# Kernel tuning notes

Hardware: AMD Instinct MI355X
Metric: run time of the kernel (lower is better)

The kernel has to match this reference:

```python
import jax, jax.numpy as jnp
import numpy as np

N, E, D, L, G = 100000, 300000, 256, 5, 4096


def _bn(x, p):
    # p: [4, dim] = (gamma, beta, running_mean, running_var); eval-mode BatchNorm1d
    g, b, m, v = p
    return (x - m) * jax.lax.rsqrt(v + 1e-5) * g + b


def setup_inputs() -> dict:
    key = jax.random.key(0)
    ks = iter(jax.random.split(key, 48))

    def nrm(shape, scale=0.02):
        return jax.random.normal(next(ks), shape, dtype=jnp.float32) * scale

    def bn_params(n, dim):
        g = 1.0 + nrm((n, dim), 0.1)
        b = nrm((n, dim), 0.1)
        m = nrm((n, dim), 0.1)
        v = 1.0 + jax.random.uniform(next(ks), (n, dim), dtype=jnp.float32)
        return jnp.stack([g, b, m, v], axis=1)  # [n,4,dim]

    return {
        "x": jax.random.randint(next(ks), (N, 9), 0, 2, dtype=jnp.int32),
        "edge_index": jax.random.randint(next(ks), (2, E), 0, N, dtype=jnp.int32),
        "edge_attr": jax.random.randint(next(ks), (E, 3), 0, 2, dtype=jnp.int32),
        "batch": jnp.sort(jax.random.randint(next(ks), (N,), 0, G, dtype=jnp.int32)),
        "atom_emb": nrm((9, 120, D)),            # AtomEncoder: 9 feature tables
        "bond_emb": nrm((L, 3, 6, D)),           # per-layer BondEncoder: 3 feature tables
        "vn0": jnp.zeros((D,), jnp.float32),     # virtualnode embedding (init 0)
        "eps": jnp.zeros((L,), jnp.float32),     # GIN eps per layer
        "conv_W1": nrm((L, D, 2 * D), 1.0 / np.sqrt(D)),     # GIN MLP (sampled BayesLinear)
        "conv_b1": nrm((L, 2 * D)),
        "conv_bn1": bn_params(L, 2 * D),
        "conv_W2": nrm((L, 2 * D, D), 1.0 / np.sqrt(2 * D)),
        "conv_b2": nrm((L, D)),
        "node_bn": bn_params(L, D),              # per-layer outer BatchNorm
        "vn_W1": nrm((L - 1, D, D), 1.0 / np.sqrt(D)),       # virtual-node MLP
        "vn_b1": nrm((L - 1, D)),
        "vn_bn1": bn_params(L - 1, D),
        "vn_W2": nrm((L - 1, D, D), 1.0 / np.sqrt(D)),
        "vn_b2": nrm((L - 1, D)),
        "vn_bn2": bn_params(L - 1, D),
    }


def reference(x, edge_index, edge_attr, batch, atom_emb, bond_emb, vn0, eps,
              conv_W1, conv_b1, conv_bn1, conv_W2, conv_b2, node_bn,
              vn_W1, vn_b1, vn_bn1, vn_W2, vn_b2, vn_bn2):
    src, dst = edge_index[0], edge_index[1]
    n_nodes = x.shape[0]
    n_layers = conv_W1.shape[0]
    # AtomEncoder: sum of 9 feature embeddings -> [N, D]
    h = atom_emb[jnp.arange(9), x].sum(axis=1)
    vn = jnp.broadcast_to(vn0, (G, vn0.shape[0]))  # [G, D]
    for l in range(n_layers):
        # broadcast virtual node into graph's nodes
        h = h + vn[batch]
        # GINConv: msg = relu(x_j + bond_emb), sum-aggregate, MLP((1+eps)x + aggr)
        e = bond_emb[l][jnp.arange(3), edge_attr].sum(axis=1)  # [E, D]
        msg = jax.nn.relu(h[src] + e)
        aggr = jax.ops.segment_sum(msg, dst, num_segments=n_nodes)
        t = (1.0 + eps[l]) * h + aggr
        t = jax.nn.relu(_bn(t @ conv_W1[l] + conv_b1[l], conv_bn1[l])) @ conv_W2[l] + conv_b2[l]
        hn = _bn(t, node_bn[l])  # outer BatchNorm (eval); dropout is identity in eval
        if l < n_layers - 1:
            hn = jax.nn.relu(hn)
            # global_add_pool of pre-conv h, then virtual-node MLP update
            vtemp = jax.ops.segment_sum(h, batch, num_segments=G) + vn
            u = jax.nn.relu(_bn(vtemp @ vn_W1[l] + vn_b1[l], vn_bn1[l]))
            vn = jax.nn.relu(_bn(u @ vn_W2[l] + vn_b2[l], vn_bn2[l]))
        h = hn
    return h  # JK == 'last'
```

## Files before the change

### kernel.cpp

```cpp
#include <hip/hip_runtime.h>

#define NN 100000
#define EE 300000
#define DD 256
#define LL 5
#define GG 4096
#define DB 512
#define MPAD 100096

typedef __attribute__((ext_vector_type(4))) float f32x4;
typedef __attribute__((ext_vector_type(8))) short s16x8;

__device__ __forceinline__ ushort f2bf(float f) {
  unsigned u = __float_as_uint(f);
  return (ushort)((u + 0x7fffu + ((u >> 16) & 1u)) >> 16);
}
__device__ __forceinline__ float b2f(ushort u) {
  return __uint_as_float(((unsigned)u) << 16);
}

__device__ __forceinline__ void gload16(const void* g, void* l) {
  __builtin_amdgcn_global_load_lds((const __attribute__((address_space(1))) void*)g,
                                   (__attribute__((address_space(3))) void*)l, 16, 0, 0);
}

__global__ void k_atom(const int* __restrict__ x, const float* __restrict__ emb,
                       const float* __restrict__ vn0, ushort* __restrict__ hvb) {
  int n = blockIdx.x * 4 + (threadIdx.x >> 6);
  if (n >= NN) return;
  int d = (threadIdx.x & 63) * 4;
  const float4 v0 = *(const float4*)&vn0[d];
  float ax = v0.x, ay = v0.y, az = v0.z, aw = v0.w;
#pragma unroll
  for (int f = 0; f < 9; ++f) {
    int v = x[n * 9 + f];
    const float4 t = *(const float4*)&emb[((size_t)(f * 120 + v)) * DD + d];
    ax += t.x; ay += t.y; az += t.z; aw += t.w;
  }
  ushort4 o; o.x = f2bf(ax); o.y = f2bf(ay); o.z = f2bf(az); o.w = f2bf(aw);
  *(ushort4*)&hvb[(size_t)n * DD + d] = o;
}

__global__ void k_vninit(const float* __restrict__ vn0, float* __restrict__ vn) {
  int i = blockIdx.x * blockDim.x + threadIdx.x;
  if (i < GG * DD) vn[i] = vn0[i & (DD - 1)];
}

__global__ void k_goff(const int* __restrict__ batch, int* __restrict__ goff) {
  int g = blockIdx.x * blockDim.x + threadIdx.x;
  if (g > GG) return;
  if (g == GG) { goff[GG] = NN; return; }
  int lo = 0, hi = NN;
  while (lo < hi) { int mid = (lo + hi) >> 1; if (batch[mid] < g) lo = mid + 1; else hi = mid; }
  goff[g] = lo;
}

__global__ void k_zero(int* __restrict__ p, int n) {
  int i = blockIdx.x * 256 + threadIdx.x;
  if (i < n) p[i] = 0;
}

__global__ void k_deg(const int* __restrict__ dst, int* __restrict__ deg) {
  int e = blockIdx.x * 256 + threadIdx.x;
  if (e < EE) atomicAdd(&deg[dst[e]], 1);
}

__global__ void k_scan1(const int* __restrict__ deg, int* __restrict__ coff,
                        int* __restrict__ bsum) {
  __shared__ int wsum[16];
  __shared__ int wpre[16];
  int lane = threadIdx.x & 63, wid = threadIdx.x >> 6;
  int i = blockIdx.x * 1024 + threadIdx.x;
  int v = (i < NN) ? deg[i] : 0;
  int xv = v;
#pragma unroll
  for (int off = 1; off < 64; off <<= 1) {
    int y = __shfl_up(xv, off);
    if (lane >= off) xv += y;
  }
  if (lane == 63) wsum[wid] = xv;
  __syncthreads();
  if (wid == 0 && lane < 16) {
    int s = wsum[lane];
    int xx = s;
#pragma unroll
    for (int off = 1; off < 16; off <<= 1) {
      int y = __shfl_up(xx, off);
      if (lane >= off) xx += y;
    }
    wpre[lane] = xx - s;
  }
  __syncthreads();
  int val = xv + wpre[wid];
  if (i < NN) coff[i + 1] = val;
  if (threadIdx.x == 1023) bsum[blockIdx.x] = val;
}

__global__ void k_scan2(int* __restrict__ bsum, int nb) {
  __shared__ int ws[2];
  int t = threadIdx.x, lane = t & 63, wid = t >> 6;
  int v = (t < nb) ? bsum[t] : 0;
  int xv = v;
#pragma unroll
  for (int off = 1; off < 64; off <<= 1) {
    int y = __shfl_up(xv, off);
    if (lane >= off) xv += y;
  }
  if (lane == 63) ws[wid] = xv;
  __syncthreads();
  int incl = xv + ((wid == 1) ? ws[0] : 0);
  if (t < nb) bsum[t] = incl - v;
}

__global__ void k_scan3(int* __restrict__ coff, const int* __restrict__ bpre) {
  int i = blockIdx.x * 1024 + threadIdx.x;
  if (i == 0) coff[0] = 0;
  if (i < NN) coff[i + 1] += bpre[i >> 10];
}

__global__ void k_eposinit(const int* __restrict__ coff, int* __restrict__ epos) {
  int n = blockIdx.x * 256 + threadIdx.x;
  if (n < NN) epos[n] = coff[n];
}

__global__ void k_scatter(const int* __restrict__ dst, int* __restrict__ epos,
                          int* __restrict__ eid) {
  int e = blockIdx.x * 256 + threadIdx.x;
  if (e < EE) { int p = atomicAdd(&epos[dst[e]], 1); eid[p] = e; }
}

__global__ void k_sort(const int* __restrict__ coff, int* __restrict__ eid) {
  int n = blockIdx.x * 256 + threadIdx.x;
  if (n >= NN) return;
  int s = coff[n], t = coff[n + 1];
  for (int i = s + 1; i < t; ++i) {
    int key = eid[i]; int j = i - 1;
    while (j >= s && eid[j] > key) { eid[j + 1] = eid[j]; --j; }
    eid[j + 1] = key;
  }
}

__global__ void k_emeta(const int* __restrict__ eid, const int* __restrict__ srcs,
                        const int* __restrict__ eattr, unsigned* __restrict__ emeta) {
  int idx = blockIdx.x * 256 + threadIdx.x;
  if (idx >= EE) return;
  int e = eid[idx];
  int s = srcs[e];
  unsigned c = (unsigned)(eattr[e * 3 + 0] + 2 * eattr[e * 3 + 1] + 4 * eattr[e * 3 + 2]);
  emeta[idx] = (unsigned)s | (c << 17);
}

__global__ void k_bond8(const float* __restrict__ bondE, float* __restrict__ bond8) {
  int l = blockIdx.x, c = blockIdx.y, d = threadIdx.x;
  float v = bondE[(((size_t)l * 3 + 0) * 6 + (c & 1)) * DD + d]
          + bondE[(((size_t)l * 3 + 1) * 6 + ((c >> 1) & 1)) * DD + d]
          + bondE[(((size_t)l * 3 + 2) * 6 + ((c >> 2) & 1)) * DD + d];
  bond8[((size_t)l * 8 + c) * DD + d] = v;
}

__global__ void k_wt(const float* __restrict__ in, ushort* __restrict__ out, int K, int N) {
  __shared__ float t[16][17];
  int l = blockIdx.z;
  int kb = blockIdx.x * 16, nb = blockIdx.y * 16;
  int tx = threadIdx.x & 15, ty = threadIdx.x >> 4;
  t[ty][tx] = in[(size_t)l * K * N + (size_t)(kb + ty) * N + nb + tx];
  __syncthreads();
  out[(size_t)l * N * K + (size_t)(nb + ty) * K + kb + tx] = f2bf(t[tx][ty]);
}

__global__ void k_pool(const ushort* __restrict__ hvb, const float* __restrict__ vn,
                       ushort* __restrict__ vtempb, const int* __restrict__ goff) {
  int g = blockIdx.x * 4 + (threadIdx.x >> 6);
  if (g >= GG) return;
  int d = (threadIdx.x & 63) * 4;
  float4 v = *(const float4*)&vn[(size_t)g * DD + d];
  float ax = v.x, ay = v.y, az = v.z, aw = v.w;
  int r0 = goff[g], r1 = goff[g + 1];
  for (int r = r0; r < r1; ++r) {
    ushort4 hu = *(const ushort4*)&hvb[(size_t)r * DD + d];
    ax += b2f(hu.x); ay += b2f(hu.y); az += b2f(hu.z); aw += b2f(hu.w);
  }
  ushort4 o; o.x = f2bf(ax); o.y = f2bf(ay); o.z = f2bf(az); o.w = f2bf(aw);
  *(ushort4*)&vtempb[(size_t)g * DD + d] = o;
}

__global__ void k_aggr(const ushort* __restrict__ hvb, ushort* __restrict__ tb,
                       const unsigned* __restrict__ emeta, const int* __restrict__ coff,
                       const float* __restrict__ bond8l, const float* __restrict__ epsp,
                       int l) {
  int n = blockIdx.x * 4 + (threadIdx.x >> 6);
  if (n >= NN) return;
  int d = (threadIdx.x & 63) * 4;
  float ax = 0.f, ay = 0.f, az = 0.f, aw = 0.f;
  int s0 = coff[n], s1 = coff[n + 1];
  int idx = s0;
  for (; idx + 2 <= s1; idx += 2) {
    unsigned m0 = emeta[idx], m1 = emeta[idx + 1];
    const ushort4 h0 = *(const ushort4*)&hvb[(size_t)(m0 & 0x1FFFFu) * DD + d];
    const ushort4 h1 = *(const ushort4*)&hvb[(size_t)(m1 & 0x1FFFFu) * DD + d];
    const float4 b0 = *(const float4*)&bond8l[(size_t)(m0 >> 17) * DD + d];
    const float4 b1 = *(const float4*)&bond8l[(size_t)(m1 >> 17) * DD + d];
    ax += fmaxf(b2f(h0.x) + b0.x, 0.f) + fmaxf(b2f(h1.x) + b1.x, 0.f);
    ay += fmaxf(b2f(h0.y) + b0.y, 0.f) + fmaxf(b2f(h1.y) + b1.y, 0.f);
    az += fmaxf(b2f(h0.z) + b0.z, 0.f) + fmaxf(b2f(h1.z) + b1.z, 0.f);
    aw += fmaxf(b2f(h0.w) + b0.w, 0.f) + fmaxf(b2f(h1.w) + b1.w, 0.f);
  }
  if (idx < s1) {
    unsigned m0 = emeta[idx];
    const ushort4 h0 = *(const ushort4*)&hvb[(size_t)(m0 & 0x1FFFFu) * DD + d];
    const float4 b0 = *(const float4*)&bond8l[(size_t)(m0 >> 17) * DD + d];
    ax += fmaxf(b2f(h0.x) + b0.x, 0.f);
    ay += fmaxf(b2f(h0.y) + b0.y, 0.f);
    az += fmaxf(b2f(h0.z) + b0.z, 0.f);
    aw += fmaxf(b2f(h0.w) + b0.w, 0.f);
  }
  float ep = 1.f + epsp[l];
  const ushort4 hn = *(const ushort4*)&hvb[(size_t)n * DD + d];
  ushort4 o;
  o.x = f2bf(ep * b2f(hn.x) + ax); o.y = f2bf(ep * b2f(hn.y) + ay);
  o.z = f2bf(ep * b2f(hn.z) + az); o.w = f2bf(ep * b2f(hn.w) + aw);
  *(ushort4*)&tb[(size_t)n * DD + d] = o;
}

__global__ __launch_bounds__(256) void k_mfma_gemm(
    const ushort* __restrict__ A, int M, int K,
    const ushort* __restrict__ BT, int N, int CT, int remap,
    void* __restrict__ Cv, int outBf16, int doRelu,
    const float* __restrict__ bias, const float* __restrict__ bn,
    const float* __restrict__ vnAdd, const int* __restrict__ batchv) {
  __shared__ ushort Asm[2][128 * 64];
  __shared__ ushort Bsm[2][128 * 64];
  int rowBase, colBase;
  if (remap) {
    const int T = gridDim.x;
    const int q = T >> 3, r = T & 7;
    const int xcd = blockIdx.x & 7, li = blockIdx.x >> 3;
    const int w0 = xcd * q + (xcd < r ? xcd : r) + li;
    rowBase = (w0 / CT) * 128;
    colBase = (w0 % CT) * 128;
  } else {
    rowBase = blockIdx.x * 128;
    colBase = blockIdx.y * 128;
  }
  const int tid = threadIdx.x;
  const int lane = tid & 63;
  const int wv = tid >> 6;
  const int wrow = (wv >> 1) * 64, wcol = (wv & 1) * 64;
  const int r16 = lane & 15, kgrp = lane >> 4;

  f32x4 acc[4][4];
#pragma unroll
  for (int m = 0; m < 4; ++m)
#pragma unroll
    for (int n = 0; n < 4; ++n) acc[m][n] = (f32x4)0.f;

  const ushort* Ap[4];
  const ushort* Bp[4];
#pragma unroll
  for (int i = 0; i < 4; ++i) {
    int c = tid + i * 256;
    int row = c >> 3, kg = (c & 7) ^ (row & 7);
    Ap[i] = A + (size_t)(rowBase + row) * K + kg * 8;
    Bp[i] = BT + (size_t)(colBase + row) * K + kg * 8;
  }

  int aoff[4][2], boff[4][2];
#pragma unroll
  for (int m = 0; m < 4; ++m) {
    int row = wrow + m * 16 + r16;
    int col = wcol + m * 16 + r16;
#pragma unroll
    for (int ks = 0; ks < 2; ++ks) {
      aoff[m][ks] = row * 128 + (((ks * 4 + kgrp) ^ (row & 7)) << 4);
      boff[m][ks] = col * 128 + (((ks * 4 + kgrp) ^ (col & 7)) << 4);
    }
  }

  const int nk = K >> 6;
  auto stage = [&](int t, int b) {
    int ko = t << 6;
#pragma unroll
    for (int i = 0; i < 4; ++i)
      gload16(Ap[i] + ko, (char*)Asm[b] + (tid + i * 256) * 16);
#pragma unroll
    for (int i = 0; i < 4; ++i)
      gload16(Bp[i] + ko, (char*)Bsm[b] + (tid + i * 256) * 16);
  };

  stage(0, 0);
  __syncthreads();
  int cur = 0;
  for (int t = 0; t < nk; ++t) {
    if (t + 1 < nk) stage(t + 1, cur ^ 1);
    const char* cA = (const char*)Asm[cur];
    const char* cB = (const char*)Bsm[cur];
#pragma unroll
    for (int ks = 0; ks < 2; ++ks) {
      s16x8 a[4], b[4];
#pragma unroll
      for (int m = 0; m < 4; ++m) a[m] = *(const s16x8*)(cA + aoff[m][ks]);
#pragma unroll
      for (int n = 0; n < 4; ++n) b[n] = *(const s16x8*)(cB + boff[n][ks]);
#pragma unroll
      for (int m = 0; m < 4; ++m)
#pragma unroll
        for (int n = 0; n < 4; ++n)
          acc[m][n] = __builtin_amdgcn_mfma_f32_16x16x32_bf16(a[m], b[n], acc[m][n], 0, 0, 0);
    }
    __syncthreads();
    cur ^= 1;
  }

  float alpha[4], beta[4];
#pragma unroll
  for (int n = 0; n < 4; ++n) {
    int col = colBase + wcol + n * 16 + r16;
    float g = bn[col], bb = bn[N + col], mm = bn[2 * N + col], vv = bn[3 * N + col];
    float s = g * rsqrtf(vv + 1e-5f);
    alpha[n] = s; beta[n] = fmaf(bias[col] - mm, s, bb);
  }
#pragma unroll
  for (int m = 0; m < 4; ++m) {
#pragma unroll
    for (int rr = 0; rr < 4; ++rr) {
      int row = rowBase + wrow + m * 16 + kgrp * 4 + rr;
      if (row < M) {
        const float* vp = vnAdd ? (vnAdd + (size_t)batchv[row] * N) : nullptr;
#pragma unroll
        for (int n = 0; n < 4; ++n) {
          int col = colBase + wcol + n * 16 + r16;
          float v = fmaf(acc[m][n][rr], alpha[n], beta[n]);
          if (doRelu) v = fmaxf(v, 0.f);
          if (vp) v += vp[col];
          if (outBf16) ((ushort*)Cv)[(size_t)row * N + col] = f2bf(v);
          else         ((float*)Cv)[(size_t)row * N + col] = v;
        }
      }
    }
  }
}

extern "C" void kernel_launch(void* const* d_in, const int* in_sizes, int n_in,
                              void* d_out, int out_size, void* d_ws, size_t ws_size,
                              hipStream_t stream) {
  const int*   x     = (const int*)d_in[0];
  const int*   ei    = (const int*)d_in[1];
  const int*   ea    = (const int*)d_in[2];
  const int*   batch = (const int*)d_in[3];
  const float* atomE = (const float*)d_in[4];
  const float* bondE = (const float*)d_in[5];
  const float* vn0   = (const float*)d_in[6];
  const float* eps   = (const float*)d_in[7];
  const float* cW1   = (const float*)d_in[8];
  const float* cb1   = (const float*)d_in[9];
  const float* cbn1  = (const float*)d_in[10];
  const float* cW2   = (const float*)d_in[11];
  const float* cb2   = (const float*)d_in[12];
  const float* nbn   = (const float*)d_in[13];
  const float* vW1   = (const float*)d_in[14];
  const float* vb1   = (const float*)d_in[15];
  const float* vbn1  = (const float*)d_in[16];
  const float* vW2   = (const float*)d_in[17];
  const float* vb2   = (const float*)d_in[18];
  const float* vbn2  = (const float*)d_in[19];
  (void)in_sizes; (void)n_in; (void)out_size; (void)ws_size;

  char* wsp = (char*)d_ws;
  size_t o = 0;
  auto alloc = [&](size_t bytes) -> char* {
    char* p = wsp + o; o += (bytes + 255) & ~(size_t)255; return p;
  };
  ushort* tbuf  = (ushort*)alloc((size_t)MPAD * DD * 2);
  ushort* c1b   = (ushort*)alloc((size_t)MPAD * DB * 2);
  float*  vn    = (float*) alloc((size_t)GG * DD * 4);
  ushort* vtmpb = (ushort*)alloc((size_t)GG * DD * 2);
  ushort* ub    = (ushort*)alloc((size_t)GG * DD * 2);
  ushort* bw1   = (ushort*)alloc((size_t)LL * DB * DD * 2);
  ushort* bw2   = (ushort*)alloc((size_t)LL * DD * DB * 2);
  ushort* bvw1  = (ushort*)alloc((size_t)(LL - 1) * DD * DD * 2);
  ushort* bvw2  = (ushort*)alloc((size_t)(LL - 1) * DD * DD * 2);
  float*  bond8 = (float*) alloc((size_t)LL * 8 * DD * 4);
  unsigned* emeta = (unsigned*)alloc((size_t)EE * 4);
  int* coff = (int*)alloc((size_t)(NN + 1) * 4);
  int* deg  = (int*)alloc((size_t)NN * 4);
  int* epos = (int*)alloc((size_t)NN * 4);
  int* eid  = (int*)alloc((size_t)EE * 4);
  int* goff = (int*)alloc((size_t)(GG + 1) * 4);
  int* bsum = (int*)alloc((size_t)128 * 4);

  const int* srcs = ei;
  const int* dsts = ei + EE;
  ushort* hvb = (ushort*)d_out;

  k_atom<<<(NN + 3) / 4, 256, 0, stream>>>(x, atomE, vn0, hvb);
  k_vninit<<<(GG * DD + 255) / 256, 256, 0, stream>>>(vn0, vn);
  k_goff<<<(GG + 256) / 256, 256, 0, stream>>>(batch, goff);
  k_zero<<<(NN + 255) / 256, 256, 0, stream>>>(deg, NN);
  k_deg<<<(EE + 255) / 256, 256, 0, stream>>>(dsts, deg);
  {
    int nb = (NN + 1023) / 1024;
    k_scan1<<<nb, 1024, 0, stream>>>(deg, coff, bsum);
    k_scan2<<<1, 128, 0, stream>>>(bsum, nb);
    k_scan3<<<nb, 1024, 0, stream>>>(coff, bsum);
  }
  k_eposinit<<<(NN + 255) / 256, 256, 0, stream>>>(coff, epos);
  k_scatter<<<(EE + 255) / 256, 256, 0, stream>>>(dsts, epos, eid);
  k_sort<<<(NN + 255) / 256, 256, 0, stream>>>(coff, eid);
  k_emeta<<<(EE + 255) / 256, 256, 0, stream>>>(eid, srcs, ea, emeta);
  k_bond8<<<dim3(LL, 8), 256, 0, stream>>>(bondE, bond8);
  k_wt<<<dim3(DD / 16, DB / 16, LL), 256, 0, stream>>>(cW1, bw1, DD, DB);
  k_wt<<<dim3(DB / 16, DD / 16, LL), 256, 0, stream>>>(cW2, bw2, DB, DD);
  k_wt<<<dim3(DD / 16, DD / 16, LL - 1), 256, 0, stream>>>(vW1, bvw1, DD, DD);
  k_wt<<<dim3(DD / 16, DD / 16, LL - 1), 256, 0, stream>>>(vW2, bvw2, DD, DD);

  for (int l = 0; l < LL; ++l) {
    if (l < LL - 1) {
      k_pool<<<(GG + 3) / 4, 256, 0, stream>>>(hvb, vn, vtmpb, goff);
      k_mfma_gemm<<<(GG / 128) * 2, 256, 0, stream>>>(
          vtmpb, GG, DD, bvw1 + (size_t)l * DD * DD, DD, 2, 1,
          ub, 1, 1, vb1 + (size_t)l * DD, vbn1 + (size_t)l * 4 * DD, nullptr, nullptr);
      k_mfma_gemm<<<(GG / 128) * 2, 256, 0, stream>>>(
          ub, GG, DD, bvw2 + (size_t)l * DD * DD, DD, 2, 1,
          vn, 0, 1, vb2 + (size_t)l * DD, vbn2 + (size_t)l * 4 * DD, nullptr, nullptr);
    }
    k_aggr<<<(NN + 3) / 4, 256, 0, stream>>>(hvb, tbuf, emeta, coff,
                                             bond8 + (size_t)l * 8 * DD, eps, l);
    k_mfma_gemm<<<(MPAD / 128) * 4, 256, 0, stream>>>(
        tbuf, NN, DD, bw1 + (size_t)l * DB * DD, DB, 4, 1,
        c1b, 1, 1, cb1 + (size_t)l * DB, cbn1 + (size_t)l * 4 * DB, nullptr, nullptr);
    if (l < LL - 1) {
      k_mfma_gemm<<<dim3(MPAD / 128, DD / 128), 256, 0, stream>>>(
          c1b, NN, DB, bw2 + (size_t)l * DD * DB, DD, 0, 0,
          hvb, 1, 1, cb2 + (size_t)l * DD, nbn + (size_t)l * 4 * DD, vn, batch);
    } else {
      k_mfma_gemm<<<dim3(MPAD / 128, DD / 128), 256, 0, stream>>>(
          c1b, NN, DB, bw2 + (size_t)l * DD * DB, DD, 0, 0,
          (float*)d_out, 0, 0, cb2 + (size_t)l * DD, nbn + (size_t)l * 4 * DD,
          nullptr, nullptr);
    }
  }
}
```

Baseline: 1.311 ms.

## Use 256x128 eight-wave MFMA GEMM tiles with triple-buffered LDS pipeline

Replaces the 128x128, 4-wave bf16 MFMA GEMM with a 256x128 tile computed by 8 waves, each owning a 128x32 sub-tile. LDS staging becomes a three-deep ring with explicit vmcnt waits and one barrier per K step, so two tiles of global loads stay in flight. MFMA bursts are wrapped in s_setprio. The second conv GEMM also gets the XCD-aware block remap. The aim is more operand reuse per LDS byte and better overlap of loads with MFMA. In exchange the kernel uses about 144KB of LDS per block, which limits occupancy to one block per CU.

```diff
diff --git a/kernel.cpp b/kernel.cpp
--- a/kernel.cpp
+++ b/kernel.cpp
@@ -222,113 +222,127 @@
   *(ushort4*)&tb[(size_t)n * DD + d] = o;
 }
 
-__global__ __launch_bounds__(256) void k_mfma_gemm(
+__global__ __launch_bounds__(512) void k_gemm8(
     const ushort* __restrict__ A, int M, int K,
     const ushort* __restrict__ BT, int N, int CT, int remap,
     void* __restrict__ Cv, int outBf16, int doRelu,
     const float* __restrict__ bias, const float* __restrict__ bn,
     const float* __restrict__ vnAdd, const int* __restrict__ batchv) {
-  __shared__ ushort Asm[2][128 * 64];
-  __shared__ ushort Bsm[2][128 * 64];
+  __shared__ ushort Asm[3][256 * 64];
+  __shared__ ushort Bsm[3][128 * 64];
   int rowBase, colBase;
   if (remap) {
     const int T = gridDim.x;
     const int q = T >> 3, r = T & 7;
     const int xcd = blockIdx.x & 7, li = blockIdx.x >> 3;
     const int w0 = xcd * q + (xcd < r ? xcd : r) + li;
-    rowBase = (w0 / CT) * 128;
+    rowBase = (w0 / CT) * 256;
     colBase = (w0 % CT) * 128;
   } else {
-    rowBase = blockIdx.x * 128;
+    rowBase = blockIdx.x * 256;
     colBase = blockIdx.y * 128;
   }
   const int tid = threadIdx.x;
   const int lane = tid & 63;
   const int wv = tid >> 6;
-  const int wrow = (wv >> 1) * 64, wcol = (wv & 1) * 64;
+  const int wr = wv >> 2, wc = wv & 3;
   const int r16 = lane & 15, kgrp = lane >> 4;
 
-  f32x4 acc[4][4];
-#pragma unroll
-  for (int m = 0; m < 4; ++m)
-#pragma unroll
-    for (int n = 0; n < 4; ++n) acc[m][n] = (f32x4)0.f;
-
-  const ushort* Ap[4];
-  const ushort* Bp[4];
+  f32x4 acc[8][2];
+#pragma unroll
+  for (int m = 0; m < 8; ++m)
+#pragma unroll
+    for (int n = 0; n < 2; ++n) acc[m][n] = (f32x4)0.f;
+
+  const ushort* ApG[4];
 #pragma unroll
   for (int i = 0; i < 4; ++i) {
-    int c = tid + i * 256;
+    int c = tid + i * 512;
     int row = c >> 3, kg = (c & 7) ^ (row & 7);
-    Ap[i] = A + (size_t)(rowBase + row) * K + kg * 8;
-    Bp[i] = BT + (size_t)(colBase + row) * K + kg * 8;
-  }
-
-  int aoff[4][2], boff[4][2];
-#pragma unroll
-  for (int m = 0; m < 4; ++m) {
-    int row = wrow + m * 16 + r16;
-    int col = wcol + m * 16 + r16;
+    ApG[i] = A + (size_t)(rowBase + row) * K + kg * 8;
+  }
+  const ushort* BpG[2];
+#pragma unroll
+  for (int i = 0; i < 2; ++i) {
+    int c = tid + i * 512;
+    int col = c >> 3, kg = (c & 7) ^ (col & 7);
+    BpG[i] = BT + (size_t)(colBase + col) * K + kg * 8;
+  }
+
+  int aoff[8][2], boff[2][2];
+#pragma unroll
+  for (int m = 0; m < 8; ++m) {
+    int row = wr * 128 + m * 16 + r16;
+#pragma unroll
+    for (int ks = 0; ks < 2; ++ks)
+      aoff[m][ks] = (row * 8 + ((ks * 4 + kgrp) ^ (row & 7))) * 16;
+  }
+#pragma unroll
+  for (int n = 0; n < 2; ++n) {
+    int col = wc * 32 + n * 16 + r16;
+#pragma unroll
+    for (int ks = 0; ks < 2; ++ks)
+      boff[n][ks] = (col * 8 + ((ks * 4 + kgrp) ^ (col & 7))) * 16;
+  }
+
+  const int nk = K >> 6;
+  auto stage = [&](int t) {
+    int b = t % 3;
+    int ko = t << 6;
+#pragma unroll
+    for (int i = 0; i < 4; ++i)
+      gload16(ApG[i] + ko, (char*)Asm[b] + (tid + i * 512) * 16);
+#pragma unroll
+    for (int i = 0; i < 2; ++i)
+      gload16(BpG[i] + ko, (char*)Bsm[b] + (tid + i * 512) * 16);
+  };
+
+  stage(0);
+  if (nk > 1) stage(1);
+
+  for (int t = 0; t < nk; ++t) {
+    if (t + 1 < nk) asm volatile("s_waitcnt vmcnt(6)" ::: "memory");
+    else            asm volatile("s_waitcnt vmcnt(0)" ::: "memory");
+    __builtin_amdgcn_s_barrier();
+    __builtin_amdgcn_sched_barrier(0);
+    if (t + 2 < nk) stage(t + 2);
+    const char* cA = (const char*)Asm[t % 3];
+    const char* cB = (const char*)Bsm[t % 3];
 #pragma unroll
     for (int ks = 0; ks < 2; ++ks) {
-      aoff[m][ks] = row * 128 + (((ks * 4 + kgrp) ^ (row & 7)) << 4);
-      boff[m][ks] = col * 128 + (((ks * 4 + kgrp) ^ (col & 7)) << 4);
+      s16x8 a[8], b[2];
+#pragma unroll
+      for (int m = 0; m < 8; ++m) a[m] = *(const s16x8*)(cA + aoff[m][ks]);
+#pragma unroll
+      for (int n = 0; n < 2; ++n) b[n] = *(const s16x8*)(cB + boff[n][ks]);
+      __builtin_amdgcn_s_setprio(1);
+#pragma unroll
+      for (int m = 0; m < 8; ++m)
+#pragma unroll
+        for (int n = 0; n < 2; ++n)
+          acc[m][n] = __builtin_amdgcn_mfma_f32_16x16x32_bf16(a[m], b[n], acc[m][n], 0, 0, 0);
+      __builtin_amdgcn_s_setprio(0);
     }
   }
 
-  const int nk = K >> 6;
-  auto stage = [&](int t, int b) {
-    int ko = t << 6;
-#pragma unroll
-    for (int i = 0; i < 4; ++i)
-      gload16(Ap[i] + ko, (char*)Asm[b] + (tid + i * 256) * 16);
-#pragma unroll
-    for (int i = 0; i < 4; ++i)
-      gload16(Bp[i] + ko, (char*)Bsm[b] + (tid + i * 256) * 16);
-  };
-
-  stage(0, 0);
-  __syncthreads();
-  int cur = 0;
-  for (int t = 0; t < nk; ++t) {
-    if (t + 1 < nk) stage(t + 1, cur ^ 1);
-    const char* cA = (const char*)Asm[cur];
-    const char* cB = (const char*)Bsm[cur];
-#pragma unroll
-    for (int ks = 0; ks < 2; ++ks) {
-      s16x8 a[4], b[4];
-#pragma unroll
-      for (int m = 0; m < 4; ++m) a[m] = *(const s16x8*)(cA + aoff[m][ks]);
-#pragma unroll
-      for (int n = 0; n < 4; ++n) b[n] = *(const s16x8*)(cB + boff[n][ks]);
-#pragma unroll
-      for (int m = 0; m < 4; ++m)
-#pragma unroll
-        for (int n = 0; n < 4; ++n)
-          acc[m][n] = __builtin_amdgcn_mfma_f32_16x16x32_bf16(a[m], b[n], acc[m][n], 0, 0, 0);
-    }
-    __syncthreads();
-    cur ^= 1;
-  }
-
-  float alpha[4], beta[4];
-#pragma unroll
-  for (int n = 0; n < 4; ++n) {
-    int col = colBase + wcol + n * 16 + r16;
+  float alpha[2], beta[2];
+#pragma unroll
+  for (int n = 0; n < 2; ++n) {
+    int col = colBase + wc * 32 + n * 16 + r16;
     float g = bn[col], bb = bn[N + col], mm = bn[2 * N + col], vv = bn[3 * N + col];
     float s = g * rsqrtf(vv + 1e-5f);
     alpha[n] = s; beta[n] = fmaf(bias[col] - mm, s, bb);
   }
 #pragma unroll
-  for (int m = 0; m < 4; ++m) {
+  for (int m = 0; m < 8; ++m) {
 #pragma unroll
     for (int rr = 0; rr < 4; ++rr) {
-      int row = rowBase + wrow + m * 16 + kgrp * 4 + rr;
+      int row = rowBase + wr * 128 + m * 16 + kgrp * 4 + rr;
       if (row < M) {
         const float* vp = vnAdd ? (vnAdd + (size_t)batchv[row] * N) : nullptr;
 #pragma unroll
-        for (int n = 0; n < 4; ++n) {
-          int col = colBase + wcol + n * 16 + r16;
+        for (int n = 0; n < 2; ++n) {
+          int col = colBase + wc * 32 + n * 16 + r16;
           float v = fmaf(acc[m][n][rr], alpha[n], beta[n]);
           if (doRelu) v = fmaxf(v, 0.f);
           if (vp) v += vp[col];
@@ -416,25 +430,25 @@
   for (int l = 0; l < LL; ++l) {
     if (l < LL - 1) {
       k_pool<<<(GG + 3) / 4, 256, 0, stream>>>(hvb, vn, vtmpb, goff);
-      k_mfma_gemm<<<(GG / 128) * 2, 256, 0, stream>>>(
-          vtmpb, GG, DD, bvw1 + (size_t)l * DD * DD, DD, 2, 1,
+      k_gemm8<<<dim3(GG / 256, DD / 128), 512, 0, stream>>>(
+          vtmpb, GG, DD, bvw1 + (size_t)l * DD * DD, DD, 2, 0,
           ub, 1, 1, vb1 + (size_t)l * DD, vbn1 + (size_t)l * 4 * DD, nullptr, nullptr);
-      k_mfma_gemm<<<(GG / 128) * 2, 256, 0, stream>>>(
-          ub, GG, DD, bvw2 + (size_t)l * DD * DD, DD, 2, 1,
+      k_gemm8<<<dim3(GG / 256, DD / 128), 512, 0, stream>>>(
+          ub, GG, DD, bvw2 + (size_t)l * DD * DD, DD, 2, 0,
           vn, 0, 1, vb2 + (size_t)l * DD, vbn2 + (size_t)l * 4 * DD, nullptr, nullptr);
     }
     k_aggr<<<(NN + 3) / 4, 256, 0, stream>>>(hvb, tbuf, emeta, coff,
                                              bond8 + (size_t)l * 8 * DD, eps, l);
-    k_mfma_gemm<<<(MPAD / 128) * 4, 256, 0, stream>>>(
+    k_gemm8<<<(MPAD / 256) * (DB / 128), 512, 0, stream>>>(
         tbuf, NN, DD, bw1 + (size_t)l * DB * DD, DB, 4, 1,
         c1b, 1, 1, cb1 + (size_t)l * DB, cbn1 + (size_t)l * 4 * DB, nullptr, nullptr);
     if (l < LL - 1) {
-      k_mfma_gemm<<<dim3(MPAD / 128, DD / 128), 256, 0, stream>>>(
-          c1b, NN, DB, bw2 + (size_t)l * DD * DB, DD, 0, 0,
+      k_gemm8<<<(MPAD / 256) * (DD / 128), 512, 0, stream>>>(
+          c1b, NN, DB, bw2 + (size_t)l * DD * DB, DD, 2, 1,
           hvb, 1, 1, cb2 + (size_t)l * DD, nbn + (size_t)l * 4 * DD, vn, batch);
     } else {
-      k_mfma_gemm<<<dim3(MPAD / 128, DD / 128), 256, 0, stream>>>(
-          c1b, NN, DB, bw2 + (size_t)l * DD * DB, DD, 0, 0,
+      k_gemm8<<<(MPAD / 256) * (DD / 128), 512, 0, stream>>>(
+          c1b, NN, DB, bw2 + (size_t)l * DD * DB, DD, 2, 1,
           (float*)d_out, 0, 0, cb2 + (size_t)l * DD, nbn + (size_t)l * 4 * DD,
           nullptr, nullptr);
     }
```

New measurement: 1.479 ms. 12.8% more time.
